# Performance work log

Hardware: AMD Instinct MI355X
Metric: run time of the kernel (lower is better)

The kernel has to match this reference:

```python
import jax, jax.numpy as jnp
import numpy as np
from jax import lax

B, IC, OC = 1, 16, 32
K, STRIDE, PAD, DIL = 3, 1, 1, 1
D = 32  # each of the 4 spatial dims


def setup_inputs() -> dict:
    key = jax.random.key(0)
    k1, k2, k3 = jax.random.split(key, 3)
    inputs = jax.random.normal(k1, (B, IC, D, D, D, D), dtype=jnp.float32)
    weight = jax.random.normal(k2, (OC, IC * K ** 4), dtype=jnp.float32)
    bias = jax.random.normal(k3, (1, OC, 1, 1, 1, 1), dtype=jnp.float32)
    return {"inputs": inputs, "weight": weight, "bias": bias}


def _conv4d(x, w_flat):
    # x: [B, IC, D1, D2, D3, D4]; w_flat: [OC, IC*K^4]
    b, c, d1, d2, d3, d4 = x.shape
    w = w_flat.reshape(OC, c, K, K, K, K)
    o1 = (d1 + 2 * PAD - DIL * (K - 1) - 1) // STRIDE + 1
    # pad only the first spatial dim; 3D conv handles the rest
    xp = jnp.pad(x, ((0, 0), (0, 0), (PAD, PAD), (0, 0), (0, 0), (0, 0)))
    out = None
    for ki in range(K):  # small fixed loop over first kernel dim
        start = ki * DIL
        xs = lax.slice_in_dim(xp, start, start + (o1 - 1) * STRIDE + 1, stride=STRIDE, axis=2)
        # [B, C, O1, D2, D3, D4] -> fold O1 into batch for a 3D conv
        xb = xs.transpose(0, 2, 1, 3, 4, 5).reshape(b * o1, c, d2, d3, d4)
        y = lax.conv_general_dilated(
            xb, w[:, :, ki],
            window_strides=(STRIDE,) * 3,
            padding=[(PAD, PAD)] * 3,
            rhs_dilation=(DIL,) * 3,
            dimension_numbers=("NCDHW", "OIDHW", "NCDHW"))
        out = y if out is None else out + y
    _, _, o2, o3, o4 = out.shape
    out = out.reshape(b, o1, OC, o2, o3, o4).transpose(0, 2, 1, 3, 4, 5)
    return out  # [B, OC, O1, O2, O3, O4]


def reference(inputs, weight, bias):
    return _conv4d(inputs, weight) + bias
```

## Files before the change

### kernel.cpp

```cpp
#include <hip/hip_runtime.h>
#include <hip/hip_bf16.h>
#include <stdint.h>


typedef __bf16 bf16x8 __attribute__((ext_vector_type(8)));
typedef float f32x16 __attribute__((ext_vector_type(16)));

#define X_IC_STRIDE 1048576
#define W_K 1296
#define SX_BYTES 52224
#define WPACK_DWORDS 23040

__device__ __forceinline__ unsigned rne_bf16(float f) {
    unsigned b = __builtin_bit_cast(unsigned, f);
    return (b + 0x7FFFu + ((b >> 16) & 1u)) >> 16;
}

__global__ void pack_w_kernel(const float* __restrict__ w, unsigned* __restrict__ wpack) {
    int D = blockIdx.x * 256 + threadIdx.x;
    if (D >= WPACK_DWORDS) return;
    int t    = D & 3;
    int lane = (D >> 2) & 63;
    int fi   = D >> 8;
    int p    = fi % 5;
    int dadb = (fi / 5) % 9;
    int g    = fi / 45;
    int kh   = lane >> 5;
    int oc   = lane & 31;
    int slot = 2 * p + kh;
    unsigned pk = 0u;
    if (slot < 9) {
        int da = dadb / 3, db = dadb % 3;
        int dc = slot / 3, dd = slot % 3;
        int koff = da * 27 + db * 9 + dc * 3 + dd;
        int ic0  = g * 8 + 2 * t;
        unsigned lo = rne_bf16(w[oc * W_K + ic0 * 81 + koff]);
        unsigned hi = rne_bf16(w[oc * W_K + (ic0 + 1) * 81 + koff]);
        pk = lo | (hi << 16);
    }
    wpack[D] = pk;
}

__global__ __launch_bounds__(256, 3) void conv4d_mfma(
    const float* __restrict__ x,
    const unsigned char* __restrict__ wpack,
    const float* __restrict__ bias,
    float* __restrict__ out)
{
    __shared__ __attribute__((aligned(16))) unsigned char lds[SX_BYTES];

    const int tid  = threadIdx.x;
    const int lane = tid & 63;
    const int wv   = tid >> 6;
    const int kh   = lane >> 5;
    const int ln   = lane & 31;

    const int blk = blockIdx.x;
    const int c0  = (blk & 7) * 4;
    const int b0  = ((blk >> 3) & 15) * 2;
    const int a0  = (blk >> 7) * 2;
    const int ai  = wv >> 1, bi = wv & 1;

    int pbase[5];
#pragma unroll
    for (int p = 0; p < 5; ++p) {
        int slot = 2 * p + kh;
        int dc = (slot >= 9) ? 2 : slot / 3;
        int dd = (slot >= 9) ? 2 : slot % 3;
        pbase[p] = dc * 544 + (ln + dd) * 16;
    }

    float bv[16];
#pragma unroll
    for (int r = 0; r < 16; ++r) bv[r] = bias[(r & 3) + 8 * (r >> 2) + 4 * kh];

    f32x16 acc[4];
#pragma unroll
    for (int ci = 0; ci < 4; ++ci)
#pragma unroll
        for (int r = 0; r < 16; ++r) acc[ci][r] = 0.f;

    bf16x8 af[5];
#pragma unroll
    for (int p = 0; p < 5; ++p)
        af[p] = *(const bf16x8*)(wpack + (size_t)p * 1024 + lane * 16);

    for (int g = 0; g < 2; ++g) {
        if (g) __syncthreads();
        for (int t = tid; t < 96 * 34; t += 256) {
            int dpr = t % 34;
            int row = t / 34;
            int rc = row % 6; int r2 = row / 6;
            int rb = r2 & 3;  int ra = r2 >> 2;
            int a_in = a0 + ra - 1, b_in = b0 + rb - 1;
            int c_in = c0 + rc - 1, d_in = dpr - 1;
            uint4 pk = make_uint4(0u, 0u, 0u, 0u);
            if ((unsigned)a_in < 32u && (unsigned)b_in < 32u &&
                (unsigned)c_in < 32u && (unsigned)d_in < 32u) {
                const float* xp = x + (size_t)(g * 8) * X_IC_STRIDE +
                                  (((a_in * 32 + b_in) * 32 + c_in) * 32 + d_in);
                unsigned u[8];
#pragma unroll
                for (int j = 0; j < 8; ++j)
                    u[j] = rne_bf16(xp[j * X_IC_STRIDE]);
                pk.x = u[0] | (u[1] << 16); pk.y = u[2] | (u[3] << 16);
                pk.z = u[4] | (u[5] << 16); pk.w = u[6] | (u[7] << 16);
            }
            *(uint4*)(lds + t * 16) = pk;
        }
        __syncthreads();

        for (int dadb = 0; dadb < 9; ++dadb) {
            const int fi  = g * 9 + dadb;
            const int nfi = (fi + 1 > 17) ? 17 : fi + 1;
            bf16x8 afn[5];
#pragma unroll
            for (int p = 0; p < 5; ++p)
                afn[p] = *(const bf16x8*)(wpack + ((size_t)nfi * 5 + p) * 1024 + lane * 16);

            const int da = dadb / 3, db = dadb % 3;
            const int ubase = ((ai + da) * 24 + (bi + db) * 6) * 544;
#pragma unroll
            for (int p = 0; p < 5; ++p) {
                const unsigned char* bp = lds + ubase + pbase[p];
#pragma unroll
                for (int ci = 0; ci < 4; ++ci) {
                    bf16x8 bfrag = *(const bf16x8*)(bp + ci * 544);
                    acc[ci] = __builtin_amdgcn_mfma_f32_32x32x16_bf16(
                        af[p], bfrag, acc[ci], 0, 0, 0);
                }
            }
#pragma unroll
            for (int p = 0; p < 5; ++p) af[p] = afn[p];
        }
    }

    const size_t sp_base = (((size_t)(a0 + ai) * 32 + (b0 + bi)) * 32 + c0);
#pragma unroll
    for (int ci = 0; ci < 4; ++ci) {
#pragma unroll
        for (int r = 0; r < 16; ++r) {
            int oc_ = (r & 3) + 8 * (r >> 2) + 4 * kh;
            out[(size_t)oc_ * X_IC_STRIDE + (sp_base + ci) * 32 + ln] = acc[ci][r] + bv[r];
        }
    }
}

extern "C" void kernel_launch(void* const* d_in, const int* in_sizes, int n_in,
                              void* d_out, int out_size, void* d_ws, size_t ws_size,
                              hipStream_t stream) {
    const float* x    = (const float*)d_in[0];
    const float* w    = (const float*)d_in[1];
    const float* bias = (const float*)d_in[2];
    float* out        = (float*)d_out;
    unsigned* wpack   = (unsigned*)d_ws;

    pack_w_kernel<<<dim3((WPACK_DWORDS + 255) / 256), dim3(256), 0, stream>>>(w, wpack);
    conv4d_mfma<<<dim3(2048), dim3(256), 0, stream>>>(
        x, (const unsigned char*)d_ws, bias, out);
}
```

Measured before the change: 274.1 us.

## Pre-pack input to channel-last bf16 and stream tiles into LDS directly

Adds a pre-pass kernel that converts the fp32 input to channel-interleaved bf16 (16 channels per 32-byte spatial element), plus a zero sentinel for padding. The conv kernel then fills its LDS tile with global_load_lds 16-byte direct loads using precomputed offsets. This removes the strided per-channel fp32 gathers and the in-loop bf16 conversion that previously ran per block. It also remaps block IDs for locality and moves the bias load after the main loop. The cost is an extra 32 MB workspace write and read, and the new path only runs when the workspace is large enough.

```diff
diff --git a/kernel.cpp b/kernel.cpp
--- a/kernel.cpp
+++ b/kernel.cpp
@@ -8,12 +8,21 @@
 
 #define X_IC_STRIDE 1048576
 #define W_K 1296
-#define SX_BYTES 52224
 #define WPACK_DWORDS 23040
+#define XPACK_OFF 98304
+#define XPACK_BYTES 33554432u
+#define ZOFF XPACK_BYTES
+#define LDS_BYTES (13 * 256 * 16)
 
 __device__ __forceinline__ unsigned rne_bf16(float f) {
     unsigned b = __builtin_bit_cast(unsigned, f);
     return (b + 0x7FFFu + ((b >> 16) & 1u)) >> 16;
+}
+
+__device__ __forceinline__ void gload_lds16(const unsigned char* g, unsigned char* s) {
+    __builtin_amdgcn_global_load_lds(
+        (const __attribute__((address_space(1))) unsigned int*)g,
+        (__attribute__((address_space(3))) unsigned int*)s, 16, 0, 0);
 }
 
 __global__ void pack_w_kernel(const float* __restrict__ w, unsigned* __restrict__ wpack) {
@@ -41,13 +50,34 @@
     wpack[D] = pk;
 }
 
+__global__ __launch_bounds__(256) void pack_x_kernel(const float* __restrict__ x,
+                                                     unsigned char* __restrict__ xpack) {
+    unsigned P = blockIdx.x * 256 + threadIdx.x;
+    unsigned u[16];
+#pragma unroll
+    for (int ic = 0; ic < 16; ++ic)
+        u[ic] = rne_bf16(x[(size_t)ic * X_IC_STRIDE + P]);
+    uint4 lo = make_uint4(u[0] | (u[1] << 16), u[2] | (u[3] << 16),
+                          u[4] | (u[5] << 16), u[6] | (u[7] << 16));
+    uint4 hi = make_uint4(u[8] | (u[9] << 16), u[10] | (u[11] << 16),
+                          u[12] | (u[13] << 16), u[14] | (u[15] << 16));
+    *(uint4*)(xpack + (size_t)P * 32) = lo;
+    *(uint4*)(xpack + (size_t)P * 32 + 16) = hi;
+    if (P == 0) {
+        *(uint4*)(xpack + ZOFF) = make_uint4(0u, 0u, 0u, 0u);
+        *(uint4*)(xpack + ZOFF + 16) = make_uint4(0u, 0u, 0u, 0u);
+    }
+}
+
+template <int XP>
 __global__ __launch_bounds__(256, 3) void conv4d_mfma(
     const float* __restrict__ x,
     const unsigned char* __restrict__ wpack,
+    const unsigned char* __restrict__ xpack,
     const float* __restrict__ bias,
     float* __restrict__ out)
 {
-    __shared__ __attribute__((aligned(16))) unsigned char lds[SX_BYTES];
+    __shared__ __attribute__((aligned(16))) unsigned char lds[LDS_BYTES];
 
     const int tid  = threadIdx.x;
     const int lane = tid & 63;
@@ -55,7 +85,8 @@
     const int kh   = lane >> 5;
     const int ln   = lane & 31;
 
-    const int blk = blockIdx.x;
+    const int bid = blockIdx.x;
+    const int blk = ((bid & 7) << 8) | (bid >> 3);
     const int c0  = (blk & 7) * 4;
     const int b0  = ((blk >> 3) & 15) * 2;
     const int a0  = (blk >> 7) * 2;
@@ -70,43 +101,65 @@
         pbase[p] = dc * 544 + (ln + dd) * 16;
     }
 
-    float bv[16];
-#pragma unroll
-    for (int r = 0; r < 16; ++r) bv[r] = bias[(r & 3) + 8 * (r >> 2) + 4 * kh];
-
-    f32x16 acc[4];
-#pragma unroll
-    for (int ci = 0; ci < 4; ++ci)
-#pragma unroll
-        for (int r = 0; r < 16; ++r) acc[ci][r] = 0.f;
-
-    bf16x8 af[5];
-#pragma unroll
-    for (int p = 0; p < 5; ++p)
-        af[p] = *(const bf16x8*)(wpack + (size_t)p * 1024 + lane * 16);
-
-    for (int g = 0; g < 2; ++g) {
-        if (g) __syncthreads();
-        for (int t = tid; t < 96 * 34; t += 256) {
+    unsigned xoff[13];
+    if (XP) {
+#pragma unroll
+        for (int it = 0; it < 13; ++it) {
+            int t   = tid + it * 256;
             int dpr = t % 34;
             int row = t / 34;
             int rc = row % 6; int r2 = row / 6;
             int rb = r2 & 3;  int ra = r2 >> 2;
             int a_in = a0 + ra - 1, b_in = b0 + rb - 1;
             int c_in = c0 + rc - 1, d_in = dpr - 1;
-            uint4 pk = make_uint4(0u, 0u, 0u, 0u);
-            if ((unsigned)a_in < 32u && (unsigned)b_in < 32u &&
-                (unsigned)c_in < 32u && (unsigned)d_in < 32u) {
-                const float* xp = x + (size_t)(g * 8) * X_IC_STRIDE +
-                                  (((a_in * 32 + b_in) * 32 + c_in) * 32 + d_in);
-                unsigned u[8];
-#pragma unroll
-                for (int j = 0; j < 8; ++j)
-                    u[j] = rne_bf16(xp[j * X_IC_STRIDE]);
-                pk.x = u[0] | (u[1] << 16); pk.y = u[2] | (u[3] << 16);
-                pk.z = u[4] | (u[5] << 16); pk.w = u[6] | (u[7] << 16);
+            bool v = ((unsigned)a_in < 32u) & ((unsigned)b_in < 32u) &
+                     ((unsigned)c_in < 32u) & ((unsigned)d_in < 32u);
+            unsigned P = (unsigned)(((a_in * 32 + b_in) * 32 + c_in) * 32 + d_in);
+            xoff[it] = v ? P * 32u : ZOFF;
+        }
+    }
+
+    f32x16 acc[4];
+#pragma unroll
+    for (int ci = 0; ci < 4; ++ci)
+#pragma unroll
+        for (int r = 0; r < 16; ++r) acc[ci][r] = 0.f;
+
+    bf16x8 af[5];
+#pragma unroll
+    for (int p = 0; p < 5; ++p)
+        af[p] = *(const bf16x8*)(wpack + (size_t)p * 1024 + lane * 16);
+
+    for (int g = 0; g < 2; ++g) {
+        if (g) __syncthreads();
+        if (XP) {
+            const int gofs = g << 4;
+#pragma unroll
+            for (int it = 0; it < 13; ++it)
+                gload_lds16(xpack + xoff[it] + gofs,
+                            lds + ((it * 256 + (wv << 6)) << 4));
+        } else {
+            for (int t = tid; t < 96 * 34; t += 256) {
+                int dpr = t % 34;
+                int row = t / 34;
+                int rc = row % 6; int r2 = row / 6;
+                int rb = r2 & 3;  int ra = r2 >> 2;
+                int a_in = a0 + ra - 1, b_in = b0 + rb - 1;
+                int c_in = c0 + rc - 1, d_in = dpr - 1;
+                uint4 pk = make_uint4(0u, 0u, 0u, 0u);
+                if ((unsigned)a_in < 32u && (unsigned)b_in < 32u &&
+                    (unsigned)c_in < 32u && (unsigned)d_in < 32u) {
+                    const float* xp = x + (size_t)(g * 8) * X_IC_STRIDE +
+                                      (((a_in * 32 + b_in) * 32 + c_in) * 32 + d_in);
+                    unsigned u[8];
+#pragma unroll
+                    for (int j = 0; j < 8; ++j)
+                        u[j] = rne_bf16(xp[j * X_IC_STRIDE]);
+                    pk.x = u[0] | (u[1] << 16); pk.y = u[2] | (u[3] << 16);
+                    pk.z = u[4] | (u[5] << 16); pk.w = u[6] | (u[7] << 16);
+                }
+                *(uint4*)(lds + t * 16) = pk;
             }
-            *(uint4*)(lds + t * 16) = pk;
         }
         __syncthreads();
 
@@ -134,6 +187,10 @@
             for (int p = 0; p < 5; ++p) af[p] = afn[p];
         }
     }
+
+    float bv[16];
+#pragma unroll
+    for (int r = 0; r < 16; ++r) bv[r] = bias[(r & 3) + 8 * (r >> 2) + 4 * kh];
 
     const size_t sp_base = (((size_t)(a0 + ai) * 32 + (b0 + bi)) * 32 + c0);
 #pragma unroll
@@ -154,8 +211,15 @@
     const float* bias = (const float*)d_in[2];
     float* out        = (float*)d_out;
     unsigned* wpack   = (unsigned*)d_ws;
+    unsigned char* xpack = (unsigned char*)d_ws + XPACK_OFF;
 
     pack_w_kernel<<<dim3((WPACK_DWORDS + 255) / 256), dim3(256), 0, stream>>>(w, wpack);
-    conv4d_mfma<<<dim3(2048), dim3(256), 0, stream>>>(
-        x, (const unsigned char*)d_ws, bias, out);
-}
+    if (ws_size >= (size_t)XPACK_OFF + XPACK_BYTES + 32) {
+        pack_x_kernel<<<dim3(4096), dim3(256), 0, stream>>>(x, xpack);
+        conv4d_mfma<1><<<dim3(2048), dim3(256), 0, stream>>>(
+            x, (const unsigned char*)d_ws, xpack, bias, out);
+    } else {
+        conv4d_mfma<0><<<dim3(2048), dim3(256), 0, stream>>>(
+            x, (const unsigned char*)d_ws, xpack, bias, out);
+    }
+}
```

Measured after the change: 267.6 us. 2.4% less time.
